# Performance work log

Measured on AMD Instinct MI355X. Metric: run time of the kernel, lower is better.

The kernel has to match this reference:

```python
import jax, jax.numpy as jnp
import numpy as np
import math

D_MODEL = 1024
D_STATE = 16
D_CONV = 4
DT_RANK = math.ceil(D_MODEL / 16)  # 64


def setup_inputs() -> dict:
    key = jax.random.key(0)
    ks = jax.random.split(key, 10)
    B, L, D, N, R = 2, 4096, D_MODEL, D_STATE, DT_RANK
    x = jax.random.normal(ks[0], (B, L, D), dtype=jnp.float32)
    # A = arange(1, N+1) repeated over D; A_log = log(A)
    A_log = jnp.log(jnp.tile(jnp.arange(1, N + 1, dtype=jnp.float32), (D, 1)))  # (D, N)
    D_param = jnp.ones((D,), dtype=jnp.float32)
    # projection weights (torch Linear convention: W @ x, W shape (out, in))
    W_dt1 = jax.random.normal(ks[1], (R, D), dtype=jnp.float32) / np.sqrt(D)   # x_proj_dt
    W_dt2 = jax.random.normal(ks[2], (D, R), dtype=jnp.float32) / np.sqrt(R)   # dt_proj weight
    # dt bias init as in _init_dt_bias
    dt0 = jnp.exp(jax.random.uniform(ks[3], (D,)) * (math.log(0.1) - math.log(0.001)) + math.log(0.001))
    b_dt = dt0 + jnp.log(-jnp.expm1(-dt0))
    W_B = jax.random.normal(ks[4], (N, D), dtype=jnp.float32) / np.sqrt(D)
    W_C = jax.random.normal(ks[5], (N, D), dtype=jnp.float32) / np.sqrt(D)
    conv_w = jax.random.normal(ks[6], (D, 1, D_CONV), dtype=jnp.float32) / np.sqrt(D_CONV)  # depthwise (O,I/g,K)
    conv_b = jax.random.normal(ks[7], (D,), dtype=jnp.float32) * 0.01
    return {"x": x, "A_log": A_log, "D_param": D_param, "W_dt1": W_dt1,
            "W_dt2": W_dt2, "b_dt": b_dt, "W_B": W_B, "W_C": W_C,
            "conv_w": conv_w, "conv_b": conv_b}


def _forward(x, A_log, D_param, W_dt1, W_dt2, b_dt, W_B, W_C, conv_w, conv_b):
    B, L, D = x.shape
    N = A_log.shape[1]
    # depthwise causal conv: torch pads both sides by d_conv-1 then slices [:L]
    # == left pad (d_conv-1), right pad 0
    xc = jax.lax.conv_general_dilated(
        jnp.swapaxes(x, 1, 2),  # (B, D, L)
        conv_w,                  # (D, 1, K)
        window_strides=(1,), padding=[(D_CONV - 1, 0)],
        dimension_numbers=("NCH", "OIH", "NCH"),
        feature_group_count=D)
    x_conv = jax.nn.silu(jnp.swapaxes(xc, 1, 2) + conv_b)  # (B, L, D)

    dt = jax.nn.softplus(jnp.einsum("bld,rd->blr", x_conv, W_dt1) @ W_dt2.T + b_dt)  # (B,L,D)
    B_ssm = jnp.einsum("bld,nd->bln", x_conv, W_B)  # (B,L,N)
    C_ssm = jnp.einsum("bld,nd->bln", x_conv, W_C)  # (B,L,N)
    A = -jnp.exp(A_log)  # (D, N)

    def step(h, inputs):
        x_t, dt_t, B_t, C_t = inputs  # (B,D),(B,D),(B,N),(B,N)
        dtA = jnp.clip(dt_t[..., None] * A[None], -10.0, 0.0)
        A_bar = jnp.clip(jnp.exp(dtA), 0.0, 0.999)               # (B,D,N)
        B_bar = jnp.clip(jnp.clip(dt_t, 0.0, 1.0)[..., None] * B_t[:, None, :], -10.0, 10.0)
        h = jnp.clip(A_bar * h + B_bar * x_t[..., None], -100.0, 100.0)
        y_t = jnp.clip(jnp.einsum("bdn,bn->bd", h, C_t) + D_param * x_t, -50.0, 50.0)
        return h, y_t

    h0 = jnp.zeros((B, D, N), dtype=x.dtype)
    xs = (jnp.swapaxes(x_conv, 0, 1), jnp.swapaxes(dt, 0, 1),
          jnp.swapaxes(B_ssm, 0, 1), jnp.swapaxes(C_ssm, 0, 1))  # leading axis L
    _, y = jax.lax.scan(step, h0, xs)  # y: (L, B, D)
    return jnp.swapaxes(y, 0, 1)


def reference(x, A_log, D_param, W_dt1, W_dt2, b_dt, W_B, W_C, conv_w, conv_b):
    return _forward(x, A_log, D_param, W_dt1, W_dt2, b_dt, W_B, W_C, conv_w, conv_b)
```

## Files before the change

kernel.cpp:

```cpp
#include <hip/hip_runtime.h>
#include <hip/hip_bf16.h>

#define BB 2
#define LL 4096
#define DD 1024
#define NN 16
#define RR 64
#define KK 4
#define ROWS 8

#define TG 8
#define NG (LL / TG)


__device__ __forceinline__ float med3f(float x, float lo, float hi) {
    return __builtin_amdgcn_fmed3f(x, lo, hi);
}

template<int CTRL>
__device__ __forceinline__ float dpp_ror(float v) {
    int r = __builtin_amdgcn_update_dpp(0, __builtin_bit_cast(int, v), CTRL, 0xf, 0xf, true);
    return __builtin_bit_cast(float, r);
}

__device__ __forceinline__ float silu_f(float z) {
    float e = __expf(-z);
    return z * __builtin_amdgcn_rcpf(1.0f + e);
}

__device__ __forceinline__ float softplus_f(float z) {
    float e = __expf(-fabsf(z));
    return fmaxf(z, 0.0f) + __logf(1.0f + e);
}

__global__ __launch_bounds__(256) void prep_kernel(
    const float* __restrict__ Wdt1, const float* __restrict__ Wdt2,
    const float* __restrict__ WB, const float* __restrict__ WC,
    float* __restrict__ Wdt1T, float* __restrict__ Wdt2T, float* __restrict__ WBCT)
{
    int i = blockIdx.x * 256 + threadIdx.x;
    if (i < 65536) {
        int k = i >> 6, r = i & 63;
        Wdt1T[i] = Wdt1[r * 1024 + k];
    }
    if (i < 65536) {
        int r = i >> 10, d = i & 1023;
        Wdt2T[i] = Wdt2[d * 64 + r];
    }
    if (i < 32768) {
        int k = i >> 5, o = i & 31;
        WBCT[i] = (o < 16) ? WB[o * 1024 + k] : WC[(o - 16) * 1024 + k];
    }
}

__global__ __launch_bounds__(256) void proj_kernel(
    const float* __restrict__ x,
    const float* __restrict__ conv_w, const float* __restrict__ conv_b,
    const float* __restrict__ Wdt1T, const float* __restrict__ Wdt2T,
    const float* __restrict__ b_dt, const float* __restrict__ WBCT,
    float2* __restrict__ xdtT, float2* __restrict__ bcT)
{
    __shared__ alignas(16) float xc8[1024 * ROWS];
    __shared__ alignas(16) float part[2048];
    __shared__ alignas(16) float dtpre[64 * ROWS];

    const int t = threadIdx.x;
    const int blk = blockIdx.x;
    const int b = blk >> 9;
    const int l0 = (blk & 511) << 3;
    const int gg = l0 >> 3;
    const float* xb = x + (size_t)b * LL * DD;

    float xc_reg[4][ROWS];
    #pragma unroll
    for (int dd = 0; dd < 4; ++dd) {
        int d = t + dd * 256;
        float4 w4 = reinterpret_cast<const float4*>(conv_w)[d];
        float cb = conv_b[d];
        float xv[ROWS + 3];
        #pragma unroll
        for (int j = 0; j < ROWS + 3; ++j) {
            int l = l0 - 3 + j;
            xv[j] = (l >= 0) ? xb[(size_t)l * DD + d] : 0.0f;
        }
        #pragma unroll
        for (int r = 0; r < ROWS; ++r) {
            float s = cb + xv[r] * w4.x + xv[r + 1] * w4.y + xv[r + 2] * w4.z + xv[r + 3] * w4.w;
            xc_reg[dd][r] = silu_f(s);
        }
        float4 lo = make_float4(xc_reg[dd][0], xc_reg[dd][1], xc_reg[dd][2], xc_reg[dd][3]);
        float4 hi = make_float4(xc_reg[dd][4], xc_reg[dd][5], xc_reg[dd][6], xc_reg[dd][7]);
        reinterpret_cast<float4*>(&xc8[d * ROWS])[0] = lo;
        reinterpret_cast<float4*>(&xc8[d * ROWS])[1] = hi;
    }
    __syncthreads();

    const float4* xr4 = reinterpret_cast<const float4*>(xc8);

    {
        int r = t & 63, seg = t >> 6;
        float acc[ROWS];
        #pragma unroll
        for (int q = 0; q < ROWS; ++q) acc[q] = 0.0f;
        const float* wp = Wdt1T + (size_t)(seg * 256) * 64 + r;
        int kbase = seg * 256;
        for (int i = 0; i < 256; ++i) {
            float wv = wp[(size_t)i * 64];
            float4 a = xr4[(kbase + i) * 2];
            float4 c = xr4[(kbase + i) * 2 + 1];
            acc[0] += a.x * wv; acc[1] += a.y * wv; acc[2] += a.z * wv; acc[3] += a.w * wv;
            acc[4] += c.x * wv; acc[5] += c.y * wv; acc[6] += c.z * wv; acc[7] += c.w * wv;
        }
        #pragma unroll
        for (int q = 0; q < ROWS; ++q) part[seg * 512 + r * 8 + q] = acc[q];
    }
    __syncthreads();
    {
        int idx = t;
        #pragma unroll
        for (int rep = 0; rep < 2; ++rep, idx += 256) {
            float s = part[idx] + part[512 + idx] + part[1024 + idx] + part[1536 + idx];
            dtpre[idx] = s;
        }
    }
    __syncthreads();

    const float4* dp4 = reinterpret_cast<const float4*>(dtpre);
    float2* xTbase = xdtT + ((size_t)b * NG + gg) * DD * TG;
    #pragma unroll
    for (int dd = 0; dd < 4; ++dd) {
        int d = t + dd * 256;
        float bd = b_dt[d];
        float acc[ROWS];
        #pragma unroll
        for (int q = 0; q < ROWS; ++q) acc[q] = bd;
        const float* wp = Wdt2T + d;
        for (int r = 0; r < 64; ++r) {
            float wv = wp[(size_t)r * 1024];
            float4 p0 = dp4[r * 2];
            float4 p1 = dp4[r * 2 + 1];
            acc[0] += p0.x * wv; acc[1] += p0.y * wv; acc[2] += p0.z * wv; acc[3] += p0.w * wv;
            acc[4] += p1.x * wv; acc[5] += p1.y * wv; acc[6] += p1.z * wv; acc[7] += p1.w * wv;
        }
        float sp[ROWS];
        #pragma unroll
        for (int row = 0; row < ROWS; ++row) sp[row] = softplus_f(acc[row]);
        float4* dst4 = (float4*)(xTbase + (size_t)d * TG);
        #pragma unroll
        for (int q = 0; q < 4; ++q)
            dst4[q] = make_float4(xc_reg[dd][2 * q], sp[2 * q],
                                  xc_reg[dd][2 * q + 1], sp[2 * q + 1]);
    }

    {
        int o = t & 31, seg = t >> 5;
        float acc[ROWS];
        #pragma unroll
        for (int q = 0; q < ROWS; ++q) acc[q] = 0.0f;
        const float* wp = WBCT + (size_t)(seg * 128) * 32 + o;
        int kbase = seg * 128;
        for (int i = 0; i < 128; ++i) {
            float wv = wp[(size_t)i * 32];
            float4 a = xr4[(kbase + i) * 2];
            float4 c = xr4[(kbase + i) * 2 + 1];
            acc[0] += a.x * wv; acc[1] += a.y * wv; acc[2] += a.z * wv; acc[3] += a.w * wv;
            acc[4] += c.x * wv; acc[5] += c.y * wv; acc[6] += c.z * wv; acc[7] += c.w * wv;
        }
        #pragma unroll
        for (int q = 0; q < ROWS; ++q) part[seg * 256 + o * 8 + q] = acc[q];
    }
    __syncthreads();
    if (t < 128) {
        int n2 = t >> 3, row = t & 7;
        float Bv = 0.0f, Cv = 0.0f;
        #pragma unroll
        for (int seg = 0; seg < 8; ++seg) {
            Bv += part[seg * 256 + n2 * 8 + row];
            Cv += part[seg * 256 + (n2 + 16) * 8 + row];
        }
        bcT[(((size_t)b * NG + gg) * NN + n2) * TG + row] = make_float2(Bv, Cv);
    }
}

struct Gran { float4 X[4]; float4 B[4]; };

__device__ __forceinline__ void gload(Gran& G, const float4* __restrict__ xq,
                                      const float4* __restrict__ bq) {
    #pragma unroll
    for (int j = 0; j < 4; ++j) G.X[j] = xq[j];
    #pragma unroll
    for (int j = 0; j < 4; ++j) G.B[j] = bq[j];
}

template<int PAR>
__device__ __forceinline__ void consume(const Gran& G, float& h, float& yr,
                                        float A2, float Dp, int n) {
    float a[TG], u[TG], Dx[TG];
    #pragma unroll
    for (int t = 0; t < TG; ++t) {
        const int j = t >> 1; const bool hf = t & 1;
        float xv = hf ? G.X[j].z : G.X[j].x;
        float dt = hf ? G.X[j].w : G.X[j].y;
        a[t] = fminf(__builtin_amdgcn_exp2f(fmaxf(dt * A2, -14.426950408889634f)), 0.999f);
        u[t] = med3f(fminf(dt, 1.0f) * (hf ? G.B[j].z : G.B[j].x), -10.0f, 10.0f) * xv;
        Dx[t] = Dp * xv;
    }
    #pragma unroll
    for (int t = 0; t < TG; ++t) {
        const int j = t >> 1; const bool hf = t & 1;
        float Cv = hf ? G.B[j].w : G.B[j].y;
        h = med3f(fmaf(a[t], h, u[t]), -100.0f, 100.0f);
        float p = h * Cv;
        p += dpp_ror<0x121>(p);
        p += dpp_ror<0x122>(p);
        p += dpp_ror<0x124>(p);
        p += dpp_ror<0x128>(p);
        float yv = med3f(p + Dx[t], -50.0f, 50.0f);
        yr = (n == PAR * TG + t) ? yv : yr;
    }
}

#define SCAN_ITER(RING, PAR, DO_STORE, LG)                                 \
    asm volatile("s_waitcnt vmcnt(24)" ::: "memory");                      \
    consume<PAR>(RING, h, yr, A2, Dp, n);                                  \
    if (DO_STORE) { *yq = yr; yq += 16 * DD; }                             \
    gload(RING, xq + (size_t)(LG) * 4096, bq + (size_t)(LG) * 64);

__global__ __launch_bounds__(64, 1) void scan_kernel(
    const float2* __restrict__ xdtT, const float2* __restrict__ bcT,
    const float* __restrict__ A_log, const float* __restrict__ Dparam,
    float* __restrict__ y)
{
    const int w = blockIdx.x;
    const int b = w >> 8;
    const int dbase = (w & 255) << 2;
    const int lane = threadIdx.x;
    const int n = lane & 15;
    const int dl = lane >> 4;
    const int d = dbase + dl;

    const float A2 = -__expf(A_log[d * NN + n]) * 1.4426950408889634f;
    const float Dp = Dparam[d];

    const float4* xq = (const float4*)(xdtT + ((size_t)b * NG * DD + d) * TG);
    const float4* bq = (const float4*)(bcT + ((size_t)b * NG * NN + n) * TG);
    float* yq = y + ((size_t)b * LL + n) * DD + dbase + dl;

    Gran r0, r1, r2, r3;
    float h = 0.0f, yr = 0.0f;

    gload(r0, xq, bq);
    gload(r1, xq + 4096, bq + 64);
    gload(r2, xq + 2 * 4096, bq + 2 * 64);
    gload(r3, xq + 3 * 4096, bq + 3 * 64);

    #pragma unroll 1
    for (int blk = 0; blk < 127; ++blk) {
        const int g4 = blk * 4;
        SCAN_ITER(r0, 0, false, g4 + 4)
        SCAN_ITER(r1, 1, true,  g4 + 5)
        SCAN_ITER(r2, 0, false, g4 + 6)
        SCAN_ITER(r3, 1, true,  g4 + 7)
    }

    asm volatile("s_waitcnt vmcnt(24)" ::: "memory");
    consume<0>(r0, h, yr, A2, Dp, n);
    asm volatile("s_waitcnt vmcnt(16)" ::: "memory");
    consume<1>(r1, h, yr, A2, Dp, n);
    *yq = yr; yq += 16 * DD;
    asm volatile("s_waitcnt vmcnt(8)" ::: "memory");
    consume<0>(r2, h, yr, A2, Dp, n);
    asm volatile("s_waitcnt vmcnt(0)" ::: "memory");
    consume<1>(r3, h, yr, A2, Dp, n);
    *yq = yr;
}

extern "C" void kernel_launch(void* const* d_in, const int* in_sizes, int n_in,
                              void* d_out, int out_size, void* d_ws, size_t ws_size,
                              hipStream_t stream) {
    const float* x      = (const float*)d_in[0];
    const float* A_log  = (const float*)d_in[1];
    const float* Dparam = (const float*)d_in[2];
    const float* W_dt1  = (const float*)d_in[3];
    const float* W_dt2  = (const float*)d_in[4];
    const float* b_dt   = (const float*)d_in[5];
    const float* W_B    = (const float*)d_in[6];
    const float* W_C    = (const float*)d_in[7];
    const float* conv_w = (const float*)d_in[8];
    const float* conv_b = (const float*)d_in[9];
    float* y = (float*)d_out;

    float* ws = (float*)d_ws;
    float2* xdtT = (float2*)ws;
    float2* bcT  = (float2*)(ws + (size_t)2 * BB * LL * DD);
    float* Wdt1T = ws + (size_t)2 * BB * LL * DD + (size_t)2 * BB * LL * NN;
    float* Wdt2T = Wdt1T + 65536;
    float* WBCT  = Wdt2T + 65536;

    prep_kernel<<<256, 256, 0, stream>>>(W_dt1, W_dt2, W_B, W_C, Wdt1T, Wdt2T, WBCT);
    proj_kernel<<<BB * (LL / ROWS), 256, 0, stream>>>(x, conv_w, conv_b, Wdt1T, Wdt2T,
                                                      b_dt, WBCT, xdtT, bcT);
    scan_kernel<<<BB * (DD / 4), 64, 0, stream>>>(xdtT, bcT, A_log, Dparam, y);
}
```

Measured before the change: 454.9 us.

## Split scan across L chunks with h-only prefix recompute; stage proj stores through LDS

The scan grid is split into four chunks along the sequence. Each chunk recomputes the hidden state from the start using a cheaper h-only update that skips the C reduction and y output, then runs the full update and writes y only for its own chunk. The aim is more waves in flight and a shorter per-wave critical path on the expensive reduction steps. The cost is redundant prefix work, which grows to most of the sequence for the last chunk. Separately, the proj kernel now stages its interleaved x/dt tile through shared memory so the global stores are coalesced, at the cost of extra barriers.

```diff
diff --git a/kernel.cpp b/kernel.cpp
--- a/kernel.cpp
+++ b/kernel.cpp
@@ -11,6 +11,8 @@
 
 #define TG 8
 #define NG (LL / TG)
+#define KC 4
+#define GPC (NG / KC)
 
 
 __device__ __forceinline__ float med3f(float x, float lo, float hi) {
@@ -125,33 +127,6 @@
     }
     __syncthreads();
 
-    const float4* dp4 = reinterpret_cast<const float4*>(dtpre);
-    float2* xTbase = xdtT + ((size_t)b * NG + gg) * DD * TG;
-    #pragma unroll
-    for (int dd = 0; dd < 4; ++dd) {
-        int d = t + dd * 256;
-        float bd = b_dt[d];
-        float acc[ROWS];
-        #pragma unroll
-        for (int q = 0; q < ROWS; ++q) acc[q] = bd;
-        const float* wp = Wdt2T + d;
-        for (int r = 0; r < 64; ++r) {
-            float wv = wp[(size_t)r * 1024];
-            float4 p0 = dp4[r * 2];
-            float4 p1 = dp4[r * 2 + 1];
-            acc[0] += p0.x * wv; acc[1] += p0.y * wv; acc[2] += p0.z * wv; acc[3] += p0.w * wv;
-            acc[4] += p1.x * wv; acc[5] += p1.y * wv; acc[6] += p1.z * wv; acc[7] += p1.w * wv;
-        }
-        float sp[ROWS];
-        #pragma unroll
-        for (int row = 0; row < ROWS; ++row) sp[row] = softplus_f(acc[row]);
-        float4* dst4 = (float4*)(xTbase + (size_t)d * TG);
-        #pragma unroll
-        for (int q = 0; q < 4; ++q)
-            dst4[q] = make_float4(xc_reg[dd][2 * q], sp[2 * q],
-                                  xc_reg[dd][2 * q + 1], sp[2 * q + 1]);
-    }
-
     {
         int o = t & 31, seg = t >> 5;
         float acc[ROWS];
@@ -180,6 +155,68 @@
         }
         bcT[(((size_t)b * NG + gg) * NN + n2) * TG + row] = make_float2(Bv, Cv);
     }
+
+    const float4* dp4 = reinterpret_cast<const float4*>(dtpre);
+    float4* xc84 = reinterpret_cast<float4*>(xc8);
+    float4* xT4 = (float4*)(xdtT + ((size_t)b * NG + gg) * DD * TG);
+
+    #pragma unroll
+    for (int dd = 0; dd < 2; ++dd) {
+        int d = t + dd * 256;
+        float bd = b_dt[d];
+        float acc[ROWS];
+        #pragma unroll
+        for (int q = 0; q < ROWS; ++q) acc[q] = bd;
+        const float* wp = Wdt2T + d;
+        for (int r = 0; r < 64; ++r) {
+            float wv = wp[(size_t)r * 1024];
+            float4 p0 = dp4[r * 2];
+            float4 p1 = dp4[r * 2 + 1];
+            acc[0] += p0.x * wv; acc[1] += p0.y * wv; acc[2] += p0.z * wv; acc[3] += p0.w * wv;
+            acc[4] += p1.x * wv; acc[5] += p1.y * wv; acc[6] += p1.z * wv; acc[7] += p1.w * wv;
+        }
+        float4* s4 = xc84 + (size_t)d * 4;
+        #pragma unroll
+        for (int q = 0; q < 4; ++q)
+            s4[q] = make_float4(xc_reg[dd][2 * q], softplus_f(acc[2 * q]),
+                                xc_reg[dd][2 * q + 1], softplus_f(acc[2 * q + 1]));
+    }
+    float sp23[2][ROWS];
+    #pragma unroll
+    for (int dd = 2; dd < 4; ++dd) {
+        int d = t + dd * 256;
+        float bd = b_dt[d];
+        float acc[ROWS];
+        #pragma unroll
+        for (int q = 0; q < ROWS; ++q) acc[q] = bd;
+        const float* wp = Wdt2T + d;
+        for (int r = 0; r < 64; ++r) {
+            float wv = wp[(size_t)r * 1024];
+            float4 p0 = dp4[r * 2];
+            float4 p1 = dp4[r * 2 + 1];
+            acc[0] += p0.x * wv; acc[1] += p0.y * wv; acc[2] += p0.z * wv; acc[3] += p0.w * wv;
+            acc[4] += p1.x * wv; acc[5] += p1.y * wv; acc[6] += p1.z * wv; acc[7] += p1.w * wv;
+        }
+        #pragma unroll
+        for (int q = 0; q < ROWS; ++q) sp23[dd - 2][q] = softplus_f(acc[q]);
+    }
+    __syncthreads();
+    #pragma unroll
+    for (int j = 0; j < 8; ++j)
+        xT4[j * 256 + t] = xc84[j * 256 + t];
+    __syncthreads();
+    #pragma unroll
+    for (int dd = 0; dd < 2; ++dd) {
+        float4* s4 = xc84 + (size_t)(t + dd * 256) * 4;
+        #pragma unroll
+        for (int q = 0; q < 4; ++q)
+            s4[q] = make_float4(xc_reg[dd + 2][2 * q], sp23[dd][2 * q],
+                                xc_reg[dd + 2][2 * q + 1], sp23[dd][2 * q + 1]);
+    }
+    __syncthreads();
+    #pragma unroll
+    for (int j = 0; j < 8; ++j)
+        xT4[2048 + j * 256 + t] = xc84[j * 256 + t];
 }
 
 struct Gran { float4 X[4]; float4 B[4]; };
@@ -220,20 +257,42 @@
     }
 }
 
+__device__ __forceinline__ void consume_h(const Gran& G, float& h, float A2) {
+    float a[TG], u[TG];
+    #pragma unroll
+    for (int t = 0; t < TG; ++t) {
+        const int j = t >> 1; const bool hf = t & 1;
+        float xv = hf ? G.X[j].z : G.X[j].x;
+        float dt = hf ? G.X[j].w : G.X[j].y;
+        a[t] = fminf(__builtin_amdgcn_exp2f(fmaxf(dt * A2, -14.426950408889634f)), 0.999f);
+        u[t] = med3f(fminf(dt, 1.0f) * (hf ? G.B[j].z : G.B[j].x), -10.0f, 10.0f) * xv;
+    }
+    #pragma unroll
+    for (int t = 0; t < TG; ++t)
+        h = med3f(fmaf(a[t], h, u[t]), -100.0f, 100.0f);
+}
+
 #define SCAN_ITER(RING, PAR, DO_STORE, LG)                                 \
     asm volatile("s_waitcnt vmcnt(24)" ::: "memory");                      \
     consume<PAR>(RING, h, yr, A2, Dp, n);                                  \
     if (DO_STORE) { *yq = yr; yq += 16 * DD; }                             \
     gload(RING, xq + (size_t)(LG) * 4096, bq + (size_t)(LG) * 64);
 
-__global__ __launch_bounds__(64, 1) void scan_kernel(
+#define H_ITER(RING, LG)                                                   \
+    asm volatile("s_waitcnt vmcnt(24)" ::: "memory");                      \
+    consume_h(RING, h, A2);                                                \
+    gload(RING, xq + (size_t)(LG) * 4096, bq + (size_t)(LG) * 64);
+
+__global__ __launch_bounds__(64, 2) void scan_kernel(
     const float2* __restrict__ xdtT, const float2* __restrict__ bcT,
     const float* __restrict__ A_log, const float* __restrict__ Dparam,
     float* __restrict__ y)
 {
     const int w = blockIdx.x;
-    const int b = w >> 8;
-    const int dbase = (w & 255) << 2;
+    const int dgrp = w & 255;
+    const int k = (w >> 8) & (KC - 1);
+    const int b = w >> 10;
+    const int dbase = dgrp << 2;
     const int lane = threadIdx.x;
     const int n = lane & 15;
     const int dl = lane >> 4;
@@ -244,7 +303,10 @@
 
     const float4* xq = (const float4*)(xdtT + ((size_t)b * NG * DD + d) * TG);
     const float4* bq = (const float4*)(bcT + ((size_t)b * NG * NN + n) * TG);
-    float* yq = y + ((size_t)b * LL + n) * DD + dbase + dl;
+    float* yq = y + ((size_t)b * LL + k * GPC * TG + n) * DD + dbase + dl;
+
+    const int p1 = k * GPC;
+    const int nb = (p1 + GPC) >> 2;
 
     Gran r0, r1, r2, r3;
     float h = 0.0f, yr = 0.0f;
@@ -255,12 +317,19 @@
     gload(r3, xq + 3 * 4096, bq + 3 * 64);
 
     #pragma unroll 1
-    for (int blk = 0; blk < 127; ++blk) {
+    for (int blk = 0; blk < nb - 1; ++blk) {
         const int g4 = blk * 4;
-        SCAN_ITER(r0, 0, false, g4 + 4)
-        SCAN_ITER(r1, 1, true,  g4 + 5)
-        SCAN_ITER(r2, 0, false, g4 + 6)
-        SCAN_ITER(r3, 1, true,  g4 + 7)
+        if (g4 < p1) {
+            H_ITER(r0, g4 + 4)
+            H_ITER(r1, g4 + 5)
+            H_ITER(r2, g4 + 6)
+            H_ITER(r3, g4 + 7)
+        } else {
+            SCAN_ITER(r0, 0, false, g4 + 4)
+            SCAN_ITER(r1, 1, true,  g4 + 5)
+            SCAN_ITER(r2, 0, false, g4 + 6)
+            SCAN_ITER(r3, 1, true,  g4 + 7)
+        }
     }
 
     asm volatile("s_waitcnt vmcnt(24)" ::: "memory");
@@ -300,5 +369,5 @@
     prep_kernel<<<256, 256, 0, stream>>>(W_dt1, W_dt2, W_B, W_C, Wdt1T, Wdt2T, WBCT);
     proj_kernel<<<BB * (LL / ROWS), 256, 0, stream>>>(x, conv_w, conv_b, Wdt1T, Wdt2T,
                                                       b_dt, WBCT, xdtT, bcT);
-    scan_kernel<<<BB * (DD / 4), 64, 0, stream>>>(xdtT, bcT, A_log, Dparam, y);
-}
+    scan_kernel<<<BB * KC * (DD / 4), 64, 0, stream>>>(xdtT, bcT, A_log, Dparam, y);
+}
```

New measurement: 451.8 us. About the same (-0.7%).
